# Optimization experiments

Measured on AMD Instinct MI355X. Metric: run time of the kernel, lower is better.

## Reference

```python
import jax, jax.numpy as jnp
import numpy as np

# Model dims (Gemma-class)
B, T, HID = 1, 3072, 2048
H, KH, D = 16, 8, 128          # q heads, kv heads, head_dim
WIN = 1024                     # sliding window
EPS = 1e-6
SEQ = 1536                     # two packed sequences of length 1536


def _rms(x, w):
    # torch nn.RMSNorm: x * rsqrt(mean(x^2) + eps) [* weight]
    var = jnp.mean(x * x, axis=-1, keepdims=True)
    y = x * jax.lax.rsqrt(var + EPS)
    return y if w is None else y * w


def _rotate_half(x):
    x1, x2 = jnp.split(x, 2, axis=-1)
    return jnp.concatenate([-x2, x1], axis=-1)


def _rope(x, cos, sin):
    # x: [B,T,h,D]; cos/sin: [B,T,rd] -> unsqueeze head dim (matches cos.unsqueeze(2))
    c = cos[:, :, None, :]
    s = sin[:, :, None, :]
    rd = cos.shape[-1]
    xr, xp = x[..., :rd], x[..., rd:]
    xr = xr * c + _rotate_half(xr) * s
    return jnp.concatenate([xr, xp], axis=-1)


def _build_mask(cu_seqlens):
    # causal & within sliding window & same packed sequence (matches _sliding_mask)
    idx = jnp.arange(T)
    seg = jnp.searchsorted(cu_seqlens, idx, side='right') - 1
    i = idx[:, None]
    j = idx[None, :]
    return (i >= j) & ((i - j) < WIN) & (seg[:, None] == seg[None, :])


def _attn_layer(x, wq, qn, k, v, wo, cos, sin, mask):
    # x: [B,T,HID]; k,v: [T,KH,D] (possibly shared from an earlier layer)
    q = _rope(_rms((x @ wq).reshape(B, T, H, D), qn), cos, sin).reshape(T, H, D)
    rep = H // k.shape[1]
    kk = jnp.repeat(k, rep, axis=1)   # GQA: repeat_interleave over head dim
    vv = jnp.repeat(v, rep, axis=1)
    s = jnp.einsum('qhd,khd->hqk', q, kk)          # scale = 1.0 (as in source)
    s = jnp.where(mask, s, jnp.asarray(-1e30, s.dtype))
    p = jax.nn.softmax(s, axis=-1)
    o = jnp.einsum('hqk,khd->qhd', p, vv).reshape(B, T, H * D)
    return o @ wo


def setup_inputs() -> dict:
    key = jax.random.key(0)
    ks = jax.random.split(key, 10)
    hidden_states = jax.random.normal(ks[0], (B, T, HID), jnp.float32)
    # RoPE tables with per-packed-sequence position resets
    pos = jnp.concatenate([jnp.arange(SEQ), jnp.arange(SEQ)]).astype(jnp.float32)
    inv = 1.0 / (10000.0 ** (jnp.arange(0, D, 2, dtype=jnp.float32) / D))
    fr = pos[:, None] * inv[None, :]
    emb = jnp.concatenate([fr, fr], axis=-1)     # [T, D]
    cos = jnp.cos(emb)[None]                     # [1, T, D]
    sin = jnp.sin(emb)[None]
    w = lambda k, sh: 0.02 * jax.random.normal(k, sh, jnp.float32)
    return {
        'hidden_states': hidden_states,
        'cos': cos, 'sin': sin,
        'wq0': w(ks[1], (HID, H * D)), 'wk0': w(ks[2], (HID, KH * D)),
        'wv0': w(ks[3], (HID, KH * D)), 'wo0': w(ks[4], (H * D, HID)),
        'qn0': 1.0 + 0.01 * jax.random.normal(ks[5], (D,), jnp.float32),
        'kn0': 1.0 + 0.01 * jax.random.normal(ks[6], (D,), jnp.float32),
        'wq1': w(ks[7], (HID, H * D)), 'wo1': w(ks[8], (H * D, HID)),
        'qn1': 1.0 + 0.01 * jax.random.normal(ks[9], (D,), jnp.float32),
        'cu_seqlens': jnp.array([0, SEQ, T], dtype=jnp.int32),
    }


def reference(hidden_states, cos, sin, wq0, wk0, wv0, wo0, qn0, kn0, wq1, wo1, qn1, cu_seqlens):
    mask = _build_mask(cu_seqlens)
    # Layer 0: source layer -> computes and stores K/V
    k = _rope(_rms((hidden_states @ wk0).reshape(B, T, KH, D), kn0), cos, sin).reshape(T, KH, D)
    v = _rms((hidden_states @ wv0).reshape(B, T, KH, D), None).reshape(T, KH, D)
    out0 = _attn_layer(hidden_states, wq0, qn0, k, v, wo0, cos, sin, mask)
    # Layer 1: KV-shared layer -> reuses layer 0's K/V (skips k/v projections)
    out1 = _attn_layer(out0, wq1, qn1, k, v, wo1, cos, sin, mask)
    return out1
```

## Files before the change

### kernel.cpp

```cpp
#include <hip/hip_runtime.h>
#include <hip/hip_bf16.h>

#define T_TOK 3072
#define HIDDEN 2048
#define NHQ 16
#define NHKV 8
#define DH 128
#define WINDOW 1024
#define KVN 1024

typedef __attribute__((ext_vector_type(4))) float f32x4;
typedef __attribute__((ext_vector_type(8))) short bf16x8;
typedef __attribute__((ext_vector_type(8))) unsigned short ushort8;
typedef __attribute__((ext_vector_type(4))) unsigned short ushort4v;

__device__ __forceinline__ unsigned short f2bf(float f) {
  union { float fv; unsigned u; } v; v.fv = f;
  unsigned r = v.u + 0x7fffu + ((v.u >> 16) & 1u);
  return (unsigned short)(r >> 16);
}
__device__ __forceinline__ float bf2f(unsigned short h) {
  union { unsigned u; float f; } v; v.u = ((unsigned)h) << 16;
  return v.f;
}
__device__ __forceinline__ void split2(float f, unsigned short& hi, unsigned short& lo) {
  hi = f2bf(f);
  lo = f2bf(f - bf2f(hi));
}

__global__ __launch_bounds__(256) void cvt_split(const float* __restrict__ x,
                                                 unsigned short* __restrict__ yh,
                                                 unsigned short* __restrict__ yl, int n) {
  int i = (blockIdx.x * 256 + threadIdx.x) * 4;
  if (i >= n) return;
  f32x4 v = *(const f32x4*)(x + i);
  ushort4v oh, ol;
#pragma unroll
  for (int j = 0; j < 4; ++j) {
    unsigned short h, l;
    split2(v[j], h, l);
    oh[j] = h; ol[j] = l;
  }
  *(ushort4v*)(yh + i) = oh;
  *(ushort4v*)(yl + i) = ol;
}

__global__ __launch_bounds__(256) void transpose_qkv(const float* __restrict__ wq0,
                                                     const float* __restrict__ wk0,
                                                     const float* __restrict__ wv0,
                                                     unsigned short* __restrict__ Wth,
                                                     unsigned short* __restrict__ Wtl) {
  __shared__ float tile[32][33];
  const int K = HIDDEN;
  int id = blockIdx.x;
  const float* W; int N, local; size_t dstoff;
  if (id < 4096)      { W = wq0; N = 2048; local = id;        dstoff = 0; }
  else if (id < 6144) { W = wk0; N = 1024; local = id - 4096; dstoff = (size_t)2048 * K; }
  else                { W = wv0; N = 1024; local = id - 6144; dstoff = (size_t)3072 * K; }
  int ntc = N / 32;
  int bn = (local % ntc) * 32, bk = (local / ntc) * 32;
  int tx = threadIdx.x & 31, ty = threadIdx.x >> 5;
#pragma unroll
  for (int i = 0; i < 4; ++i)
    tile[ty + i * 8][tx] = W[(size_t)(bk + ty + i * 8) * N + bn + tx];
  __syncthreads();
#pragma unroll
  for (int i = 0; i < 4; ++i) {
    unsigned short h, l;
    split2(tile[tx][ty + i * 8], h, l);
    Wth[dstoff + (size_t)(bn + ty + i * 8) * K + bk + tx] = h;
    Wtl[dstoff + (size_t)(bn + ty + i * 8) * K + bk + tx] = l;
  }
}

__global__ __launch_bounds__(256) void transpose_w_split(const float* __restrict__ W,
                                                         unsigned short* __restrict__ Wth,
                                                         unsigned short* __restrict__ Wtl,
                                                         int K, int N) {
  __shared__ float tile[32][33];
  int bn = blockIdx.x * 32, bk = blockIdx.y * 32;
  int tx = threadIdx.x & 31, ty = threadIdx.x >> 5;
#pragma unroll
  for (int i = 0; i < 4; ++i)
    tile[ty + i * 8][tx] = W[(size_t)(bk + ty + i * 8) * N + bn + tx];
  __syncthreads();
#pragma unroll
  for (int i = 0; i < 4; ++i) {
    unsigned short h, l;
    split2(tile[tx][ty + i * 8], h, l);
    Wth[(size_t)(bn + ty + i * 8) * K + bk + tx] = h;
    if (Wtl) Wtl[(size_t)(bn + ty + i * 8) * K + bk + tx] = l;
  }
}

__global__ __launch_bounds__(256) void transpose_u16(const unsigned short* __restrict__ src,
                                                     unsigned short* __restrict__ dst,
                                                     int R, int C) {
  __shared__ unsigned short tile[32][33];
  int bc = blockIdx.x * 32, br = blockIdx.y * 32;
  int tx = threadIdx.x & 31, ty = threadIdx.x >> 5;
#pragma unroll
  for (int i = 0; i < 4; ++i)
    tile[ty + i * 8][tx] = src[(size_t)(br + ty + i * 8) * C + bc + tx];
  __syncthreads();
#pragma unroll
  for (int i = 0; i < 4; ++i)
    dst[(size_t)(bc + ty + i * 8) * R + br + tx] = tile[tx][ty + i * 8];
}

#define GSLOT(lane) ((((lane) & 3) + 4 - (((lane) >> 3) & 3)) & 3)

template <int OUT>
__global__ __launch_bounds__(256) void gemm3_128(const unsigned short* __restrict__ Ah,
                                                 const unsigned short* __restrict__ Al,
                                                 const unsigned short* __restrict__ Bh,
                                                 const unsigned short* __restrict__ Bl,
                                                 float* __restrict__ Cq,
                                                 float* __restrict__ Ckv,
                                                 unsigned short* __restrict__ Ch,
                                                 unsigned short* __restrict__ Cl,
                                                 int strd, int M, int N, int K) {
  __shared__ unsigned short ah_lds[128 * 32];
  __shared__ unsigned short al_lds[128 * 32];
  __shared__ unsigned short bh_lds[128 * 32];
  __shared__ unsigned short bl_lds[128 * 32];
  const int tid = threadIdx.x, lane = tid & 63, wave = tid >> 6;
  const int wr = (wave >> 1) * 64, wc = (wave & 1) * 64;
  const int g = lane >> 4, r16 = lane & 15;
  int nwg = gridDim.x * gridDim.y;
  int id = blockIdx.y * gridDim.x + blockIdx.x;
  int nid = (id & 7) * (nwg >> 3) + (id >> 3);
  const int bm = nid % gridDim.x, bn = nid / gridDim.x;
  f32x4 acc[4][4];
#pragma unroll
  for (int i = 0; i < 4; ++i)
#pragma unroll
    for (int j = 0; j < 4; ++j) acc[i][j] = (f32x4){0.f, 0.f, 0.f, 0.f};

  const unsigned short* AhB = Ah + (size_t)bm * 128 * K;
  const unsigned short* AlB = Al + (size_t)bm * 128 * K;
  const unsigned short* BhB = Bh + (size_t)bn * 128 * K;
  const unsigned short* BlB = Bl + (size_t)bn * 128 * K;

  const int slg = GSLOT(lane) * 8;
  const int sr = ((r16 >> 1) & 3);

  for (int kt = 0; kt < K; kt += 32) {
    __syncthreads();
#pragma unroll
    for (int c = 0; c < 2; ++c) {
      size_t goff = (size_t)(wave * 32 + c * 16 + (lane >> 2)) * K + kt + slg;
      int loff = (wave * 2 + c) * 512;
      __builtin_amdgcn_global_load_lds(
          (const __attribute__((address_space(1))) unsigned int*)(AhB + goff),
          (__attribute__((address_space(3))) unsigned int*)(ah_lds + loff), 16, 0, 0);
      __builtin_amdgcn_global_load_lds(
          (const __attribute__((address_space(1))) unsigned int*)(AlB + goff),
          (__attribute__((address_space(3))) unsigned int*)(al_lds + loff), 16, 0, 0);
      __builtin_amdgcn_global_load_lds(
          (const __attribute__((address_space(1))) unsigned int*)(BhB + goff),
          (__attribute__((address_space(3))) unsigned int*)(bh_lds + loff), 16, 0, 0);
      __builtin_amdgcn_global_load_lds(
          (const __attribute__((address_space(1))) unsigned int*)(BlB + goff),
          (__attribute__((address_space(3))) unsigned int*)(bl_lds + loff), 16, 0, 0);
    }
    __syncthreads();
    bf16x8 ahf[4], alf[4], bhf[4], blf[4];
    int sa = ((g + sr) & 3) * 8;
#pragma unroll
    for (int i = 0; i < 4; ++i) {
      ahf[i] = *(const bf16x8*)&ah_lds[(wr + i * 16 + r16) * 32 + sa];
      alf[i] = *(const bf16x8*)&al_lds[(wr + i * 16 + r16) * 32 + sa];
      bhf[i] = *(const bf16x8*)&bh_lds[(wc + i * 16 + r16) * 32 + sa];
      blf[i] = *(const bf16x8*)&bl_lds[(wc + i * 16 + r16) * 32 + sa];
    }
#pragma unroll
    for (int i = 0; i < 4; ++i)
#pragma unroll
      for (int j = 0; j < 4; ++j) {
        acc[i][j] = __builtin_amdgcn_mfma_f32_16x16x32_bf16(ahf[i], bhf[j], acc[i][j], 0, 0, 0);
        acc[i][j] = __builtin_amdgcn_mfma_f32_16x16x32_bf16(ahf[i], blf[j], acc[i][j], 0, 0, 0);
        acc[i][j] = __builtin_amdgcn_mfma_f32_16x16x32_bf16(alf[i], bhf[j], acc[i][j], 0, 0, 0);
      }
  }

#pragma unroll
  for (int i = 0; i < 4; ++i) {
    int row = bm * 128 + wr + i * 16 + g * 4;
#pragma unroll
    for (int j = 0; j < 4; ++j) {
      int colg = bn * 128 + wc + j * 16 + r16;
      if (OUT == 0) {
        float* Cb; int cc;
        if (colg < 2048) { Cb = Cq; cc = colg; } else { Cb = Ckv; cc = colg - 2048; }
#pragma unroll
        for (int r = 0; r < 4; ++r)
          Cb[(size_t)(row + r) * strd + cc] = acc[i][j][r];
      } else {
#pragma unroll
        for (int r = 0; r < 4; ++r) {
          unsigned short h, l;
          split2(acc[i][j][r], h, l);
          Ch[(size_t)(row + r) * N + colg] = h;
          Cl[(size_t)(row + r) * N + colg] = l;
        }
      }
    }
  }
}

__global__ __launch_bounds__(256) void gemm3_96(const unsigned short* __restrict__ Ah,
                                                const unsigned short* __restrict__ Al,
                                                const unsigned short* __restrict__ Bh,
                                                const unsigned short* __restrict__ Bl,
                                                float* __restrict__ Cf,
                                                int M, int N, int K) {
  __shared__ unsigned short ah_lds[96 * 32];
  __shared__ unsigned short al_lds[96 * 32];
  __shared__ unsigned short bh_lds[128 * 32];
  __shared__ unsigned short bl_lds[128 * 32];
  const int tid = threadIdx.x, lane = tid & 63, wave = tid >> 6;
  const int wr = (wave >> 1) * 48, wc = (wave & 1) * 64;
  const int g = lane >> 4, r16 = lane & 15;
  int nwg = gridDim.x * gridDim.y;
  int id = blockIdx.y * gridDim.x + blockIdx.x;
  int nid = (id & 7) * (nwg >> 3) + (id >> 3);
  const int bm = nid % gridDim.x, bn = nid / gridDim.x;
  f32x4 acc[3][4];
#pragma unroll
  for (int i = 0; i < 3; ++i)
#pragma unroll
    for (int j = 0; j < 4; ++j) acc[i][j] = (f32x4){0.f, 0.f, 0.f, 0.f};

  const unsigned short* AhB = Ah + (size_t)bm * 96 * K;
  const unsigned short* AlB = Al + (size_t)bm * 96 * K;
  const unsigned short* BhB = Bh + (size_t)bn * 128 * K;
  const unsigned short* BlB = Bl + (size_t)bn * 128 * K;

  const int slg = GSLOT(lane) * 8;
  const int sr = ((r16 >> 1) & 3);

  for (int kt = 0; kt < K; kt += 32) {
    __syncthreads();
    {
      int c = wave;
      size_t goff = (size_t)(c * 16 + (lane >> 2)) * K + kt + slg;
      __builtin_amdgcn_global_load_lds(
          (const __attribute__((address_space(1))) unsigned int*)(AhB + goff),
          (__attribute__((address_space(3))) unsigned int*)(ah_lds + c * 512), 16, 0, 0);
      __builtin_amdgcn_global_load_lds(
          (const __attribute__((address_space(1))) unsigned int*)(AlB + goff),
          (__attribute__((address_space(3))) unsigned int*)(al_lds + c * 512), 16, 0, 0);
      if (wave < 2) {
        int c2 = 4 + wave;
        size_t goff2 = (size_t)(c2 * 16 + (lane >> 2)) * K + kt + slg;
        __builtin_amdgcn_global_load_lds(
            (const __attribute__((address_space(1))) unsigned int*)(AhB + goff2),
            (__attribute__((address_space(3))) unsigned int*)(ah_lds + c2 * 512), 16, 0, 0);
        __builtin_amdgcn_global_load_lds(
            (const __attribute__((address_space(1))) unsigned int*)(AlB + goff2),
            (__attribute__((address_space(3))) unsigned int*)(al_lds + c2 * 512), 16, 0, 0);
      }
    }
#pragma unroll
    for (int c = 0; c < 2; ++c) {
      size_t goff = (size_t)(wave * 32 + c * 16 + (lane >> 2)) * K + kt + slg;
      int loff = (wave * 2 + c) * 512;
      __builtin_amdgcn_global_load_lds(
          (const __attribute__((address_space(1))) unsigned int*)(BhB + goff),
          (__attribute__((address_space(3))) unsigned int*)(bh_lds + loff), 16, 0, 0);
      __builtin_amdgcn_global_load_lds(
          (const __attribute__((address_space(1))) unsigned int*)(BlB + goff),
          (__attribute__((address_space(3))) unsigned int*)(bl_lds + loff), 16, 0, 0);
    }
    __syncthreads();
    bf16x8 ahf[3], alf[3], bhf[4], blf[4];
    int sa = ((g + sr) & 3) * 8;
#pragma unroll
    for (int i = 0; i < 3; ++i) {
      ahf[i] = *(const bf16x8*)&ah_lds[(wr + i * 16 + r16) * 32 + sa];
      alf[i] = *(const bf16x8*)&al_lds[(wr + i * 16 + r16) * 32 + sa];
    }
#pragma unroll
    for (int j = 0; j < 4; ++j) {
      bhf[j] = *(const bf16x8*)&bh_lds[(wc + j * 16 + r16) * 32 + sa];
      blf[j] = *(const bf16x8*)&bl_lds[(wc + j * 16 + r16) * 32 + sa];
    }
#pragma unroll
    for (int i = 0; i < 3; ++i)
#pragma unroll
      for (int j = 0; j < 4; ++j) {
        acc[i][j] = __builtin_amdgcn_mfma_f32_16x16x32_bf16(ahf[i], bhf[j], acc[i][j], 0, 0, 0);
        acc[i][j] = __builtin_amdgcn_mfma_f32_16x16x32_bf16(ahf[i], blf[j], acc[i][j], 0, 0, 0);
        acc[i][j] = __builtin_amdgcn_mfma_f32_16x16x32_bf16(alf[i], bhf[j], acc[i][j], 0, 0, 0);
      }
  }

#pragma unroll
  for (int i = 0; i < 3; ++i) {
    int row = bm * 96 + wr + i * 16 + g * 4;
#pragma unroll
    for (int j = 0; j < 4; ++j) {
      int col = bn * 128 + wc + j * 16 + r16;
#pragma unroll
      for (int r = 0; r < 4; ++r)
        Cf[(size_t)(row + r) * N + col] = acc[i][j][r];
    }
  }
}

__global__ __launch_bounds__(256) void gemm1_96(const unsigned short* __restrict__ Ah,
                                                const unsigned short* __restrict__ Bh,
                                                float* __restrict__ Cf,
                                                int M, int N, int K) {
  __shared__ unsigned short ah_lds[96 * 32];
  __shared__ unsigned short bh_lds[128 * 32];
  const int tid = threadIdx.x, lane = tid & 63, wave = tid >> 6;
  const int wr = (wave >> 1) * 48, wc = (wave & 1) * 64;
  const int g = lane >> 4, r16 = lane & 15;
  int nwg = gridDim.x * gridDim.y;
  int id = blockIdx.y * gridDim.x + blockIdx.x;
  int nid = (id & 7) * (nwg >> 3) + (id >> 3);
  const int bm = nid % gridDim.x, bn = nid / gridDim.x;
  f32x4 acc[3][4];
#pragma unroll
  for (int i = 0; i < 3; ++i)
#pragma unroll
    for (int j = 0; j < 4; ++j) acc[i][j] = (f32x4){0.f, 0.f, 0.f, 0.f};

  const unsigned short* AhB = Ah + (size_t)bm * 96 * K;
  const unsigned short* BhB = Bh + (size_t)bn * 128 * K;

  const int slg = GSLOT(lane) * 8;
  const int sr = ((r16 >> 1) & 3);

  for (int kt = 0; kt < K; kt += 32) {
    __syncthreads();
    {
      int c = wave;
      size_t goff = (size_t)(c * 16 + (lane >> 2)) * K + kt + slg;
      __builtin_amdgcn_global_load_lds(
          (const __attribute__((address_space(1))) unsigned int*)(AhB + goff),
          (__attribute__((address_space(3))) unsigned int*)(ah_lds + c * 512), 16, 0, 0);
      if (wave < 2) {
        int c2 = 4 + wave;
        size_t goff2 = (size_t)(c2 * 16 + (lane >> 2)) * K + kt + slg;
        __builtin_amdgcn_global_load_lds(
            (const __attribute__((address_space(1))) unsigned int*)(AhB + goff2),
            (__attribute__((address_space(3))) unsigned int*)(ah_lds + c2 * 512), 16, 0, 0);
      }
    }
#pragma unroll
    for (int c = 0; c < 2; ++c) {
      size_t goff = (size_t)(wave * 32 + c * 16 + (lane >> 2)) * K + kt + slg;
      __builtin_amdgcn_global_load_lds(
          (const __attribute__((address_space(1))) unsigned int*)(BhB + goff),
          (__attribute__((address_space(3))) unsigned int*)(bh_lds + (wave * 2 + c) * 512), 16, 0, 0);
    }
    __syncthreads();
    bf16x8 ahf[3], bhf[4];
    int sa = ((g + sr) & 3) * 8;
#pragma unroll
    for (int i = 0; i < 3; ++i)
      ahf[i] = *(const bf16x8*)&ah_lds[(wr + i * 16 + r16) * 32 + sa];
#pragma unroll
    for (int j = 0; j < 4; ++j)
      bhf[j] = *(const bf16x8*)&bh_lds[(wc + j * 16 + r16) * 32 + sa];
#pragma unroll
    for (int i = 0; i < 3; ++i)
#pragma unroll
      for (int j = 0; j < 4; ++j)
        acc[i][j] = __builtin_amdgcn_mfma_f32_16x16x32_bf16(ahf[i], bhf[j], acc[i][j], 0, 0, 0);
  }

#pragma unroll
  for (int i = 0; i < 3; ++i) {
    int row = bm * 96 + wr + i * 16 + g * 4;
#pragma unroll
    for (int j = 0; j < 4; ++j) {
      int col = bn * 128 + wc + j * 16 + r16;
#pragma unroll
      for (int r = 0; r < 4; ++r)
        Cf[(size_t)(row + r) * N + col] = acc[i][j][r];
    }
  }
}

__global__ __launch_bounds__(256) void rms_kv(const float* __restrict__ X,
                                              const float* __restrict__ kn,
                                              const float* __restrict__ cosp,
                                              const float* __restrict__ sinp,
                                              unsigned short* __restrict__ kh,
                                              unsigned short* __restrict__ kl,
                                              unsigned short* __restrict__ vh) {
  const int half = T_TOK * NHKV / 4;
  bool isV = (int)blockIdx.x >= half;
  int bid = isV ? blockIdx.x - half : blockIdx.x;
  int row = bid * 4 + (threadIdx.x >> 6);
  int lane = threadIdx.x & 63;
  int t = row >> 3, hh_ = row & 7;
  const float* x = X + (size_t)t * HIDDEN + (isV ? KVN : 0) + (size_t)hh_ * DH;
  float x1 = x[lane], x2 = x[lane + 64];
  float ss = x1 * x1 + x2 * x2;
#pragma unroll
  for (int m = 1; m < 64; m <<= 1) ss += __shfl_xor(ss, m, 64);
  float inv = rsqrtf(ss * (1.0f / 128.0f) + 1e-6f);
  float y1 = x1 * inv, y2 = x2 * inv;
  if (!isV) {
    y1 *= kn[lane]; y2 *= kn[lane + 64];
    float c1 = cosp[t * DH + lane], s1 = sinp[t * DH + lane];
    float c2 = cosp[t * DH + lane + 64], s2 = sinp[t * DH + lane + 64];
    float o1 = y1 * c1 - y2 * s1;
    float o2 = y2 * c2 + y1 * s2;
    unsigned short h, l;
    split2(o1, h, l);
    kh[(size_t)row * DH + lane] = h;
    kl[(size_t)row * DH + lane] = l;
    split2(o2, h, l);
    kh[(size_t)row * DH + lane + 64] = h;
    kl[(size_t)row * DH + lane + 64] = l;
  } else {
    vh[(size_t)row * DH + lane] = f2bf(y1);
    vh[(size_t)row * DH + lane + 64] = f2bf(y2);
  }
}

template <int WRITE_LO>
__global__ __launch_bounds__(384) void attn3(const float* __restrict__ Qf,
                                             const float* __restrict__ qnw,
                                             const float* __restrict__ cosp,
                                             const float* __restrict__ sinp,
                                             const unsigned short* __restrict__ Kh,
                                             const unsigned short* __restrict__ Kl,
                                             const unsigned short* __restrict__ Vth,
                                             unsigned short* __restrict__ Oh,
                                             unsigned short* __restrict__ Ol,
                                             const int* __restrict__ cu, int ncu) {
  __shared__ unsigned short kh_lds[32][136];
  __shared__ unsigned short kl_lds[32][136];
  __shared__ unsigned short vh_lds[144][40];
  __shared__ unsigned short ph_lds[6][16][40];

  int id = blockIdx.y * gridDim.x + blockIdx.x;
  int nid = (id & 7) * 64 + (id >> 3);
  const int qt = nid & 31, h = nid >> 5;
  const int qbase = qt * 96;
  const int kvh = h >> 1;
  const int tid = threadIdx.x, lane = tid & 63, wave = tid >> 6;
  const int g = lane >> 4, r16 = lane & 15;

  for (int i = tid; i < 16 * 40; i += 384) {
    int rr = i / 40, cc = i % 40;
    vh_lds[128 + rr][cc] = (rr == 0) ? (unsigned short)0x3F80 : (unsigned short)0;
  }

  bf16x8 aqh[4], aql[4];
  {
    int q_r = qbase + wave * 16 + r16;
    const float* xq = Qf + (size_t)q_r * HIDDEN + h * DH;
    float xv[4][8];
    float ss = 0.f;
#pragma unroll
    for (int ks = 0; ks < 4; ++ks) {
      f32x4 a = *(const f32x4*)(xq + ks * 32 + g * 8);
      f32x4 b = *(const f32x4*)(xq + ks * 32 + g * 8 + 4);
#pragma unroll
      for (int j = 0; j < 4; ++j) { xv[ks][j] = a[j]; xv[ks][4 + j] = b[j]; }
#pragma unroll
      for (int j = 0; j < 8; ++j) ss += xv[ks][j] * xv[ks][j];
    }
    ss += __shfl_xor(ss, 16, 64);
    ss += __shfl_xor(ss, 32, 64);
    float inv = rsqrtf(ss * (1.0f / 128.0f) + 1e-6f);
    float y[4][8];
#pragma unroll
    for (int ks = 0; ks < 4; ++ks) {
      f32x4 w0 = *(const f32x4*)(qnw + ks * 32 + g * 8);
      f32x4 w1 = *(const f32x4*)(qnw + ks * 32 + g * 8 + 4);
#pragma unroll
      for (int j = 0; j < 4; ++j) {
        y[ks][j] = xv[ks][j] * inv * w0[j];
        y[ks][4 + j] = xv[ks][4 + j] * inv * w1[j];
      }
    }
    const float* cb = cosp + (size_t)q_r * DH;
    const float* sb = sinp + (size_t)q_r * DH;
#pragma unroll
    for (int ks = 0; ks < 4; ++ks) {
      bf16x8 th, tl;
#pragma unroll
      for (int j2 = 0; j2 < 2; ++j2) {
        int col = ks * 32 + g * 8 + j2 * 4;
        f32x4 cv = *(const f32x4*)(cb + col);
        f32x4 sv = *(const f32x4*)(sb + col);
#pragma unroll
        for (int j = 0; j < 4; ++j) {
          float o;
          if (ks < 2) o = y[ks][j2 * 4 + j] * cv[j] - y[ks + 2][j2 * 4 + j] * sv[j];
          else        o = y[ks][j2 * 4 + j] * cv[j] + y[ks - 2][j2 * 4 + j] * sv[j];
          unsigned short hx, lx;
          split2(o, hx, lx);
          th[j2 * 4 + j] = (short)hx;
          tl[j2 * 4 + j] = (short)lx;
        }
      }
      aqh[ks] = th; aql[ks] = tl;
    }
  }

  int ssr[4];
#pragma unroll
  for (int r = 0; r < 4; ++r) {
    int q_r = qbase + wave * 16 + g * 4 + r;
    int s = 0;
    for (int i = 1; i < ncu; ++i) { int v = cu[i]; if (v <= q_r) s = v; }
    ssr[r] = s;
  }
  int ss_base = 0;
  for (int i = 1; i < ncu; ++i) { int v = cu[i]; if (v <= qbase) ss_base = v; }

  float m_r[4] = {-1e30f, -1e30f, -1e30f, -1e30f};
  f32x4 oacc[8];
#pragma unroll
  for (int db = 0; db < 8; ++db) oacc[db] = (f32x4){0.f, 0.f, 0.f, 0.f};
  f32x4 oaccL = (f32x4){0.f, 0.f, 0.f, 0.f};

  int lo = qbase - WINDOW + 1;
  if (lo < ss_base) lo = ss_base;
  if (lo < 0) lo = 0;
  int kt0 = lo & ~31;
  int ktend = qbase + 95;

  const bool stager = tid < 256;
  const int krow = (tid & 255) >> 3, kc = tid & 7;
  const int vd = (tid & 255) >> 1, vhalf = (tid & 1) * 16;
  const int qmin = qbase + wave * 16;
  const int sw0 = ((kc + 2 * (krow & 15)) & 15) * 16;
  const int sw1 = ((kc + 8 + 2 * (krow & 15)) & 15) * 16;

  ushort8 rkh0, rkh1, rkl0, rkl1, rvh0, rvh1;
  auto loadTile = [&](int kt) {
    if (!stager) return;
    size_t goff = ((size_t)(kt + krow) * NHKV + kvh) * DH + kc * 8;
    rkh0 = *(const ushort8*)(Kh + goff);
    rkh1 = *(const ushort8*)(Kh + goff + 64);
    rkl0 = *(const ushort8*)(Kl + goff);
    rkl1 = *(const ushort8*)(Kl + goff + 64);
    size_t voff = ((size_t)kvh * DH + vd) * T_TOK + kt + vhalf;
    rvh0 = *(const ushort8*)(Vth + voff);
    rvh1 = *(const ushort8*)(Vth + voff + 8);
  };
  auto writeTile = [&]() {
    if (!stager) return;
    char* kbh = (char*)&kh_lds[krow][0];
    char* kbl = (char*)&kl_lds[krow][0];
    *(ushort8*)(kbh + sw0) = rkh0;
    *(ushort8*)(kbh + sw1) = rkh1;
    *(ushort8*)(kbl + sw0) = rkl0;
    *(ushort8*)(kbl + sw1) = rkl1;
    *(ushort8*)&vh_lds[vd][vhalf] = rvh0;
    *(ushort8*)&vh_lds[vd][vhalf + 8] = rvh1;
  };

  loadTile(kt0);
  writeTile();
  __syncthreads();

  for (int kt = kt0; kt <= ktend; kt += 32) {
    const bool hasNext = (kt + 32 <= ktend);
    if (hasNext) loadTile(kt + 32);

    f32x4 s0 = (f32x4){0.f, 0.f, 0.f, 0.f}, s1 = (f32x4){0.f, 0.f, 0.f, 0.f};
    {
      const char* kb0h = (const char*)&kh_lds[r16][0];
      const char* kb1h = (const char*)&kh_lds[16 + r16][0];
      const char* kb0l = (const char*)&kl_lds[r16][0];
      const char* kb1l = (const char*)&kl_lds[16 + r16][0];
#pragma unroll
      for (int ks = 0; ks < 4; ++ks) {
        int sl = ((ks * 4 + g + 2 * r16) & 15) * 16;
        bf16x8 bh0 = *(const bf16x8*)(kb0h + sl);
        bf16x8 bh1 = *(const bf16x8*)(kb1h + sl);
        bf16x8 bl0 = *(const bf16x8*)(kb0l + sl);
        bf16x8 bl1 = *(const bf16x8*)(kb1l + sl);
        s0 = __builtin_amdgcn_mfma_f32_16x16x32_bf16(aqh[ks], bh0, s0, 0, 0, 0);
        s0 = __builtin_amdgcn_mfma_f32_16x16x32_bf16(aqh[ks], bl0, s0, 0, 0, 0);
        s0 = __builtin_amdgcn_mfma_f32_16x16x32_bf16(aql[ks], bh0, s0, 0, 0, 0);
        s1 = __builtin_amdgcn_mfma_f32_16x16x32_bf16(aqh[ks], bh1, s1, 0, 0, 0);
        s1 = __builtin_amdgcn_mfma_f32_16x16x32_bf16(aqh[ks], bl1, s1, 0, 0, 0);
        s1 = __builtin_amdgcn_mfma_f32_16x16x32_bf16(aql[ks], bh1, s1, 0, 0, 0);
      }
    }

    float sv0_[4], sv1_[4], mt_[4];
    bool ok0_[4], ok1_[4];
    bool interior = (kt + 31 <= qmin) && (kt >= qmin + 16 - WINDOW) &&
                    __all(kt >= ssr[3]);
    if (interior) {
#pragma unroll
      for (int r = 0; r < 4; ++r) {
        ok0_[r] = ok1_[r] = true;
        sv0_[r] = s0[r]; sv1_[r] = s1[r];
      }
    } else {
#pragma unroll
      for (int r = 0; r < 4; ++r) {
        int q_r = qmin + g * 4 + r;
        int k0 = kt + r16, k1 = k0 + 16;
        ok0_[r] = (k0 <= q_r) && (k0 > q_r - WINDOW) && (k0 >= ssr[r]);
        ok1_[r] = (k1 <= q_r) && (k1 > q_r - WINDOW) && (k1 >= ssr[r]);
        sv0_[r] = ok0_[r] ? s0[r] : -1e30f;
        sv1_[r] = ok1_[r] ? s1[r] : -1e30f;
      }
    }
#pragma unroll
    for (int r = 0; r < 4; ++r) {
      float mt = fmaxf(sv0_[r], sv1_[r]);
#pragma unroll
      for (int mm = 1; mm < 16; mm <<= 1) mt = fmaxf(mt, __shfl_xor(mt, mm, 64));
      mt_[r] = mt;
    }
    float grow = fmaxf(fmaxf(mt_[0] - m_r[0], mt_[1] - m_r[1]),
                       fmaxf(mt_[2] - m_r[2], mt_[3] - m_r[3]));
    if (!__all(grow <= 8.0f)) {
#pragma unroll
      for (int r = 0; r < 4; ++r) {
        float mnew = fmaxf(m_r[r], mt_[r]);
        float alpha = __expf(m_r[r] - mnew);
        m_r[r] = mnew;
#pragma unroll
        for (int db = 0; db < 8; ++db) oacc[db][r] *= alpha;
        oaccL[r] *= alpha;
      }
    }
#pragma unroll
    for (int r = 0; r < 4; ++r) {
      float p0v = ok0_[r] ? __expf(sv0_[r] - m_r[r]) : 0.f;
      float p1v = ok1_[r] ? __expf(sv1_[r] - m_r[r]) : 0.f;
      ph_lds[wave][g * 4 + r][r16] = f2bf(p0v);
      ph_lds[wave][g * 4 + r][16 + r16] = f2bf(p1v);
    }

    bf16x8 pah = *(const bf16x8*)&ph_lds[wave][r16][g * 8];
#pragma unroll
    for (int db = 0; db < 8; ++db) {
      bf16x8 vfh = *(const bf16x8*)&vh_lds[db * 16 + r16][g * 8];
      oacc[db] = __builtin_amdgcn_mfma_f32_16x16x32_bf16(pah, vfh, oacc[db], 0, 0, 0);
    }
    {
      bf16x8 vfo = *(const bf16x8*)&vh_lds[128 + r16][g * 8];
      oaccL = __builtin_amdgcn_mfma_f32_16x16x32_bf16(pah, vfo, oaccL, 0, 0, 0);
    }

    __syncthreads();
    if (hasNext) writeTile();
    __syncthreads();
  }

#pragma unroll
  for (int r = 0; r < 4; ++r) {
    int q_r = qbase + wave * 16 + g * 4 + r;
    float lsum = __shfl(oaccL[r], lane & 48, 64);
    float invl = 1.f / lsum;
#pragma unroll
    for (int db = 0; db < 8; ++db) {
      float ov = oacc[db][r] * invl;
      unsigned short hh, ll;
      split2(ov, hh, ll);
      Oh[(size_t)q_r * (NHQ * DH) + h * DH + db * 16 + r16] = hh;
      if (WRITE_LO) Ol[(size_t)q_r * (NHQ * DH) + h * DH + db * 16 + r16] = ll;
    }
  }
}

extern "C" void kernel_launch(void* const* d_in, const int* in_sizes, int n_in,
                              void* d_out, int out_size, void* d_ws, size_t ws_size,
                              hipStream_t stream) {
  const float* hidden = (const float*)d_in[0];
  const float* cosp   = (const float*)d_in[1];
  const float* sinp   = (const float*)d_in[2];
  const float* wq0    = (const float*)d_in[3];
  const float* wk0    = (const float*)d_in[4];
  const float* wv0    = (const float*)d_in[5];
  const float* wo0    = (const float*)d_in[6];
  const float* qn0    = (const float*)d_in[7];
  const float* kn0    = (const float*)d_in[8];
  const float* wq1    = (const float*)d_in[9];
  const float* wo1    = (const float*)d_in[10];
  const float* qn1    = (const float*)d_in[11];
  const int*   cu     = (const int*)d_in[12];
  int ncu = in_sizes[12];
  (void)n_in; (void)out_size; (void)ws_size;

  const int nX = T_TOK * HIDDEN;

  char* p = (char*)d_ws;
  auto alloc = [&](size_t bytes) { char* r = p; p += (bytes + 255) & ~255ull; return r; };

  float*          c32q  = (float*)alloc((size_t)T_TOK * HIDDEN * 4);
  float*          c32kv = (float*)alloc((size_t)T_TOK * HIDDEN * 4);
  unsigned short* xh    = (unsigned short*)alloc((size_t)T_TOK * HIDDEN * 2);
  unsigned short* xl    = (unsigned short*)alloc((size_t)T_TOK * HIDDEN * 2);
  unsigned short* wth   = (unsigned short*)alloc((size_t)2 * HIDDEN * HIDDEN * 2);
  unsigned short* wtl   = (unsigned short*)alloc((size_t)2 * HIDDEN * HIDDEN * 2);
  unsigned short* kh    = (unsigned short*)alloc((size_t)T_TOK * KVN * 2);
  unsigned short* kl    = (unsigned short*)alloc((size_t)T_TOK * KVN * 2);
  unsigned short* vh    = (unsigned short*)alloc((size_t)T_TOK * KVN * 2);
  unsigned short* vth   = (unsigned short*)alloc((size_t)T_TOK * KVN * 2);

  unsigned short* wo0sh = wth;
  unsigned short* wo0sl = wtl;
  unsigned short* wq1th = wth + (size_t)HIDDEN * HIDDEN;
  unsigned short* wq1tl = wtl + (size_t)HIDDEN * HIDDEN;
  unsigned short* W01th = (unsigned short*)c32q;
  unsigned short* W01tl = W01th + (size_t)HIDDEN * HIDDEN;
  unsigned short* wo1t  = wth;

  cvt_split<<<nX / 1024, 256, 0, stream>>>(hidden, xh, xl, nX);

  transpose_qkv<<<8192, 256, 0, stream>>>(wq0, wk0, wv0, wth, wtl);

  gemm3_128<0><<<dim3(T_TOK / 128, 4096 / 128), 256, 0, stream>>>(
      xh, xl, wth, wtl, c32q, c32kv, nullptr, nullptr, HIDDEN, T_TOK, 4096, HIDDEN);

  cvt_split<<<(HIDDEN * HIDDEN) / 1024, 256, 0, stream>>>(wo0, wo0sh, wo0sl, HIDDEN * HIDDEN);

  transpose_w_split<<<dim3(HIDDEN / 32, HIDDEN / 32), 256, 0, stream>>>(wq1, wq1th, wq1tl, HIDDEN, HIDDEN);

  rms_kv<<<2 * T_TOK * NHKV / 4, 256, 0, stream>>>(c32kv, kn0, cosp, sinp, kh, kl, vh);

  transpose_u16<<<dim3(KVN / 32, T_TOK / 32), 256, 0, stream>>>(vh, vth, T_TOK, KVN);

  attn3<1><<<dim3(32, 16), 384, 0, stream>>>(c32q, qn0, cosp, sinp, kh, kl, vth, xh, xl, cu, ncu);

  gemm3_128<2><<<dim3(HIDDEN / 128, HIDDEN / 128), 256, 0, stream>>>(
      wq1th, wq1tl, wo0sh, wo0sl, nullptr, nullptr, W01th, W01tl, HIDDEN, HIDDEN, HIDDEN, HIDDEN);

  gemm3_96<<<dim3(T_TOK / 96, HIDDEN / 128), 256, 0, stream>>>(
      xh, xl, W01th, W01tl, c32kv, T_TOK, HIDDEN, HIDDEN);

  transpose_w_split<<<dim3(HIDDEN / 32, HIDDEN / 32), 256, 0, stream>>>(wo1, wo1t, nullptr, HIDDEN, HIDDEN);

  attn3<0><<<dim3(32, 16), 384, 0, stream>>>(c32kv, qn1, cosp, sinp, kh, kl, vth, xh, nullptr, cu, ncu);

  gemm1_96<<<dim3(T_TOK / 96, HIDDEN / 128), 256, 0, stream>>>(xh, wo1t, (float*)d_out, T_TOK, HIDDEN, HIDDEN);
}
```

Measured before the change: 666.6 us.

## Give each attention wave two 16-row query tiles, 128-row blocks with 256 threads

The attention kernel now processes 128 query rows per block with 4 waves of 256 threads, each wave handling two 16-row query sub-tiles instead of one. Every K/V tile loaded into LDS is reused across twice as many query rows per wave, and all threads now take part in staging (previously a third of the threads idled during loads). The cost is about double the accumulator registers per wave, which lowers occupancy, and a smaller grid of 384 blocks, which may underfill the 256 CUs.

After: 795.3 us. 19.3% more time.

```diff
diff --git a/kernel.cpp b/kernel.cpp
--- a/kernel.cpp
+++ b/kernel.cpp
@@ -426,7 +426,7 @@
 }
 
 template <int WRITE_LO>
-__global__ __launch_bounds__(384) void attn3(const float* __restrict__ Qf,
+__global__ __launch_bounds__(256) void attn3(const float* __restrict__ Qf,
                                              const float* __restrict__ qnw,
                                              const float* __restrict__ cosp,
                                              const float* __restrict__ sinp,
@@ -439,24 +439,25 @@
   __shared__ unsigned short kh_lds[32][136];
   __shared__ unsigned short kl_lds[32][136];
   __shared__ unsigned short vh_lds[144][40];
-  __shared__ unsigned short ph_lds[6][16][40];
+  __shared__ unsigned short ph_lds[4][32][40];
 
   int id = blockIdx.y * gridDim.x + blockIdx.x;
-  int nid = (id & 7) * 64 + (id >> 3);
-  const int qt = nid & 31, h = nid >> 5;
-  const int qbase = qt * 96;
+  int nid = (id & 7) * 48 + (id >> 3);
+  const int qt = nid % 24, h = nid / 24;
+  const int qbase = qt * 128;
   const int kvh = h >> 1;
   const int tid = threadIdx.x, lane = tid & 63, wave = tid >> 6;
   const int g = lane >> 4, r16 = lane & 15;
 
-  for (int i = tid; i < 16 * 40; i += 384) {
+  for (int i = tid; i < 16 * 40; i += 256) {
     int rr = i / 40, cc = i % 40;
     vh_lds[128 + rr][cc] = (rr == 0) ? (unsigned short)0x3F80 : (unsigned short)0;
   }
 
-  bf16x8 aqh[4], aql[4];
-  {
-    int q_r = qbase + wave * 16 + r16;
+  bf16x8 aqh[2][4], aql[2][4];
+#pragma unroll
+  for (int hf = 0; hf < 2; ++hf) {
+    int q_r = qbase + wave * 32 + hf * 16 + r16;
     const float* xq = Qf + (size_t)q_r * HIDDEN + h * DH;
     float xv[4][8];
     float ss = 0.f;
@@ -472,15 +473,14 @@
     ss += __shfl_xor(ss, 16, 64);
     ss += __shfl_xor(ss, 32, 64);
     float inv = rsqrtf(ss * (1.0f / 128.0f) + 1e-6f);
-    float y[4][8];
 #pragma unroll
     for (int ks = 0; ks < 4; ++ks) {
       f32x4 w0 = *(const f32x4*)(qnw + ks * 32 + g * 8);
       f32x4 w1 = *(const f32x4*)(qnw + ks * 32 + g * 8 + 4);
 #pragma unroll
       for (int j = 0; j < 4; ++j) {
-        y[ks][j] = xv[ks][j] * inv * w0[j];
-        y[ks][4 + j] = xv[ks][4 + j] * inv * w1[j];
+        xv[ks][j] = xv[ks][j] * inv * w0[j];
+        xv[ks][4 + j] = xv[ks][4 + j] * inv * w1[j];
       }
     }
     const float* cb = cosp + (size_t)q_r * DH;
@@ -496,51 +496,59 @@
 #pragma unroll
         for (int j = 0; j < 4; ++j) {
           float o;
-          if (ks < 2) o = y[ks][j2 * 4 + j] * cv[j] - y[ks + 2][j2 * 4 + j] * sv[j];
-          else        o = y[ks][j2 * 4 + j] * cv[j] + y[ks - 2][j2 * 4 + j] * sv[j];
+          if (ks < 2) o = xv[ks][j2 * 4 + j] * cv[j] - xv[ks + 2][j2 * 4 + j] * sv[j];
+          else        o = xv[ks][j2 * 4 + j] * cv[j] + xv[ks - 2][j2 * 4 + j] * sv[j];
           unsigned short hx, lx;
           split2(o, hx, lx);
           th[j2 * 4 + j] = (short)hx;
           tl[j2 * 4 + j] = (short)lx;
         }
       }
-      aqh[ks] = th; aql[ks] = tl;
-    }
-  }
-
-  int ssr[4];
-#pragma unroll
-  for (int r = 0; r < 4; ++r) {
-    int q_r = qbase + wave * 16 + g * 4 + r;
-    int s = 0;
-    for (int i = 1; i < ncu; ++i) { int v = cu[i]; if (v <= q_r) s = v; }
-    ssr[r] = s;
-  }
+      aqh[hf][ks] = th; aql[hf][ks] = tl;
+    }
+  }
+
+  int ssr[2][4];
+#pragma unroll
+  for (int hf = 0; hf < 2; ++hf)
+#pragma unroll
+    for (int r = 0; r < 4; ++r) {
+      int q_r = qbase + wave * 32 + hf * 16 + g * 4 + r;
+      int s = 0;
+      for (int i = 1; i < ncu; ++i) { int v = cu[i]; if (v <= q_r) s = v; }
+      ssr[hf][r] = s;
+    }
   int ss_base = 0;
   for (int i = 1; i < ncu; ++i) { int v = cu[i]; if (v <= qbase) ss_base = v; }
 
-  float m_r[4] = {-1e30f, -1e30f, -1e30f, -1e30f};
-  f32x4 oacc[8];
-#pragma unroll
-  for (int db = 0; db < 8; ++db) oacc[db] = (f32x4){0.f, 0.f, 0.f, 0.f};
-  f32x4 oaccL = (f32x4){0.f, 0.f, 0.f, 0.f};
+  float m_r[2][4];
+#pragma unroll
+  for (int hf = 0; hf < 2; ++hf)
+#pragma unroll
+    for (int r = 0; r < 4; ++r) m_r[hf][r] = -1e30f;
+  f32x4 oaccA[8], oaccB[8];
+#pragma unroll
+  for (int db = 0; db < 8; ++db) {
+    oaccA[db] = (f32x4){0.f, 0.f, 0.f, 0.f};
+    oaccB[db] = (f32x4){0.f, 0.f, 0.f, 0.f};
+  }
+  f32x4 oaccLA = (f32x4){0.f, 0.f, 0.f, 0.f};
+  f32x4 oaccLB = (f32x4){0.f, 0.f, 0.f, 0.f};
 
   int lo = qbase - WINDOW + 1;
   if (lo < ss_base) lo = ss_base;
   if (lo < 0) lo = 0;
   int kt0 = lo & ~31;
-  int ktend = qbase + 95;
-
-  const bool stager = tid < 256;
-  const int krow = (tid & 255) >> 3, kc = tid & 7;
-  const int vd = (tid & 255) >> 1, vhalf = (tid & 1) * 16;
-  const int qmin = qbase + wave * 16;
+  int ktend = qbase + 127;
+
+  const int krow = tid >> 3, kc = tid & 7;
+  const int vd = tid >> 1, vhalf = (tid & 1) * 16;
+  const int qmin = qbase + wave * 32;
   const int sw0 = ((kc + 2 * (krow & 15)) & 15) * 16;
   const int sw1 = ((kc + 8 + 2 * (krow & 15)) & 15) * 16;
 
   ushort8 rkh0, rkh1, rkl0, rkl1, rvh0, rvh1;
   auto loadTile = [&](int kt) {
-    if (!stager) return;
     size_t goff = ((size_t)(kt + krow) * NHKV + kvh) * DH + kc * 8;
     rkh0 = *(const ushort8*)(Kh + goff);
     rkh1 = *(const ushort8*)(Kh + goff + 64);
@@ -551,7 +559,6 @@
     rvh1 = *(const ushort8*)(Vth + voff + 8);
   };
   auto writeTile = [&]() {
-    if (!stager) return;
     char* kbh = (char*)&kh_lds[krow][0];
     char* kbl = (char*)&kl_lds[krow][0];
     *(ushort8*)(kbh + sw0) = rkh0;
@@ -570,7 +577,8 @@
     const bool hasNext = (kt + 32 <= ktend);
     if (hasNext) loadTile(kt + 32);
 
-    f32x4 s0 = (f32x4){0.f, 0.f, 0.f, 0.f}, s1 = (f32x4){0.f, 0.f, 0.f, 0.f};
+    f32x4 s0a = (f32x4){0.f, 0.f, 0.f, 0.f}, s1a = (f32x4){0.f, 0.f, 0.f, 0.f};
+    f32x4 s0b = (f32x4){0.f, 0.f, 0.f, 0.f}, s1b = (f32x4){0.f, 0.f, 0.f, 0.f};
     {
       const char* kb0h = (const char*)&kh_lds[r16][0];
       const char* kb1h = (const char*)&kh_lds[16 + r16][0];
@@ -583,73 +591,94 @@
         bf16x8 bh1 = *(const bf16x8*)(kb1h + sl);
         bf16x8 bl0 = *(const bf16x8*)(kb0l + sl);
         bf16x8 bl1 = *(const bf16x8*)(kb1l + sl);
-        s0 = __builtin_amdgcn_mfma_f32_16x16x32_bf16(aqh[ks], bh0, s0, 0, 0, 0);
-        s0 = __builtin_amdgcn_mfma_f32_16x16x32_bf16(aqh[ks], bl0, s0, 0, 0, 0);
-        s0 = __builtin_amdgcn_mfma_f32_16x16x32_bf16(aql[ks], bh0, s0, 0, 0, 0);
-        s1 = __builtin_amdgcn_mfma_f32_16x16x32_bf16(aqh[ks], bh1, s1, 0, 0, 0);
-        s1 = __builtin_amdgcn_mfma_f32_16x16x32_bf16(aqh[ks], bl1, s1, 0, 0, 0);
-        s1 = __builtin_amdgcn_mfma_f32_16x16x32_bf16(aql[ks], bh1, s1, 0, 0, 0);
-      }
-    }
-
-    float sv0_[4], sv1_[4], mt_[4];
-    bool ok0_[4], ok1_[4];
-    bool interior = (kt + 31 <= qmin) && (kt >= qmin + 16 - WINDOW) &&
-                    __all(kt >= ssr[3]);
-    if (interior) {
+        s0a = __builtin_amdgcn_mfma_f32_16x16x32_bf16(aqh[0][ks], bh0, s0a, 0, 0, 0);
+        s0a = __builtin_amdgcn_mfma_f32_16x16x32_bf16(aqh[0][ks], bl0, s0a, 0, 0, 0);
+        s0a = __builtin_amdgcn_mfma_f32_16x16x32_bf16(aql[0][ks], bh0, s0a, 0, 0, 0);
+        s1a = __builtin_amdgcn_mfma_f32_16x16x32_bf16(aqh[0][ks], bh1, s1a, 0, 0, 0);
+        s1a = __builtin_amdgcn_mfma_f32_16x16x32_bf16(aqh[0][ks], bl1, s1a, 0, 0, 0);
+        s1a = __builtin_amdgcn_mfma_f32_16x16x32_bf16(aql[0][ks], bh1, s1a, 0, 0, 0);
+        s0b = __builtin_amdgcn_mfma_f32_16x16x32_bf16(aqh[1][ks], bh0, s0b, 0, 0, 0);
+        s0b = __builtin_amdgcn_mfma_f32_16x16x32_bf16(aqh[1][ks], bl0, s0b, 0, 0, 0);
+        s0b = __builtin_amdgcn_mfma_f32_16x16x32_bf16(aql[1][ks], bh0, s0b, 0, 0, 0);
+        s1b = __builtin_amdgcn_mfma_f32_16x16x32_bf16(aqh[1][ks], bh1, s1b, 0, 0, 0);
+        s1b = __builtin_amdgcn_mfma_f32_16x16x32_bf16(aqh[1][ks], bl1, s1b, 0, 0, 0);
+        s1b = __builtin_amdgcn_mfma_f32_16x16x32_bf16(aql[1][ks], bh1, s1b, 0, 0, 0);
+      }
+    }
+
+#pragma unroll
+    for (int hf = 0; hf < 2; ++hf) {
+      f32x4 s0 = hf ? s0b : s0a;
+      f32x4 s1 = hf ? s1b : s1a;
+      float sv0_[4], sv1_[4], mt_[4];
+      bool ok0_[4], ok1_[4];
+      int qminh = qmin + hf * 16;
+      bool interior = (kt + 31 <= qminh) && (kt >= qminh + 16 - WINDOW) &&
+                      __all(kt >= ssr[hf][3]);
+      if (interior) {
+#pragma unroll
+        for (int r = 0; r < 4; ++r) {
+          ok0_[r] = ok1_[r] = true;
+          sv0_[r] = s0[r]; sv1_[r] = s1[r];
+        }
+      } else {
+#pragma unroll
+        for (int r = 0; r < 4; ++r) {
+          int q_r = qminh + g * 4 + r;
+          int k0 = kt + r16, k1 = k0 + 16;
+          ok0_[r] = (k0 <= q_r) && (k0 > q_r - WINDOW) && (k0 >= ssr[hf][r]);
+          ok1_[r] = (k1 <= q_r) && (k1 > q_r - WINDOW) && (k1 >= ssr[hf][r]);
+          sv0_[r] = ok0_[r] ? s0[r] : -1e30f;
+          sv1_[r] = ok1_[r] ? s1[r] : -1e30f;
+        }
+      }
 #pragma unroll
       for (int r = 0; r < 4; ++r) {
-        ok0_[r] = ok1_[r] = true;
-        sv0_[r] = s0[r]; sv1_[r] = s1[r];
-      }
-    } else {
+        float mt = fmaxf(sv0_[r], sv1_[r]);
+#pragma unroll
+        for (int mm = 1; mm < 16; mm <<= 1) mt = fmaxf(mt, __shfl_xor(mt, mm, 64));
+        mt_[r] = mt;
+      }
+      float grow = fmaxf(fmaxf(mt_[0] - m_r[hf][0], mt_[1] - m_r[hf][1]),
+                         fmaxf(mt_[2] - m_r[hf][2], mt_[3] - m_r[hf][3]));
+      if (!__all(grow <= 8.0f)) {
+#pragma unroll
+        for (int r = 0; r < 4; ++r) {
+          float mnew = fmaxf(m_r[hf][r], mt_[r]);
+          float alpha = __expf(m_r[hf][r] - mnew);
+          m_r[hf][r] = mnew;
+          if (hf == 0) {
+#pragma unroll
+            for (int db = 0; db < 8; ++db) oaccA[db][r] *= alpha;
+            oaccLA[r] *= alpha;
+          } else {
+#pragma unroll
+            for (int db = 0; db < 8; ++db) oaccB[db][r] *= alpha;
+            oaccLB[r] *= alpha;
+          }
+        }
+      }
 #pragma unroll
       for (int r = 0; r < 4; ++r) {
-        int q_r = qmin + g * 4 + r;
-        int k0 = kt + r16, k1 = k0 + 16;
-        ok0_[r] = (k0 <= q_r) && (k0 > q_r - WINDOW) && (k0 >= ssr[r]);
-        ok1_[r] = (k1 <= q_r) && (k1 > q_r - WINDOW) && (k1 >= ssr[r]);
-        sv0_[r] = ok0_[r] ? s0[r] : -1e30f;
-        sv1_[r] = ok1_[r] ? s1[r] : -1e30f;
-      }
-    }
-#pragma unroll
-    for (int r = 0; r < 4; ++r) {
-      float mt = fmaxf(sv0_[r], sv1_[r]);
-#pragma unroll
-      for (int mm = 1; mm < 16; mm <<= 1) mt = fmaxf(mt, __shfl_xor(mt, mm, 64));
-      mt_[r] = mt;
-    }
-    float grow = fmaxf(fmaxf(mt_[0] - m_r[0], mt_[1] - m_r[1]),
-                       fmaxf(mt_[2] - m_r[2], mt_[3] - m_r[3]));
-    if (!__all(grow <= 8.0f)) {
-#pragma unroll
-      for (int r = 0; r < 4; ++r) {
-        float mnew = fmaxf(m_r[r], mt_[r]);
-        float alpha = __expf(m_r[r] - mnew);
-        m_r[r] = mnew;
-#pragma unroll
-        for (int db = 0; db < 8; ++db) oacc[db][r] *= alpha;
-        oaccL[r] *= alpha;
-      }
-    }
-#pragma unroll
-    for (int r = 0; r < 4; ++r) {
-      float p0v = ok0_[r] ? __expf(sv0_[r] - m_r[r]) : 0.f;
-      float p1v = ok1_[r] ? __expf(sv1_[r] - m_r[r]) : 0.f;
-      ph_lds[wave][g * 4 + r][r16] = f2bf(p0v);
-      ph_lds[wave][g * 4 + r][16 + r16] = f2bf(p1v);
-    }
-
-    bf16x8 pah = *(const bf16x8*)&ph_lds[wave][r16][g * 8];
+        float p0v = ok0_[r] ? __expf(sv0_[r] - m_r[hf][r]) : 0.f;
+        float p1v = ok1_[r] ? __expf(sv1_[r] - m_r[hf][r]) : 0.f;
+        ph_lds[wave][hf * 16 + g * 4 + r][r16] = f2bf(p0v);
+        ph_lds[wave][hf * 16 + g * 4 + r][16 + r16] = f2bf(p1v);
+      }
+    }
+
+    bf16x8 pa0 = *(const bf16x8*)&ph_lds[wave][r16][g * 8];
+    bf16x8 pa1 = *(const bf16x8*)&ph_lds[wave][16 + r16][g * 8];
 #pragma unroll
     for (int db = 0; db < 8; ++db) {
       bf16x8 vfh = *(const bf16x8*)&vh_lds[db * 16 + r16][g * 8];
-      oacc[db] = __builtin_amdgcn_mfma_f32_16x16x32_bf16(pah, vfh, oacc[db], 0, 0, 0);
+      oaccA[db] = __builtin_amdgcn_mfma_f32_16x16x32_bf16(pa0, vfh, oaccA[db], 0, 0, 0);
+      oaccB[db] = __builtin_amdgcn_mfma_f32_16x16x32_bf16(pa1, vfh, oaccB[db], 0, 0, 0);
     }
     {
       bf16x8 vfo = *(const bf16x8*)&vh_lds[128 + r16][g * 8];
-      oaccL = __builtin_amdgcn_mfma_f32_16x16x32_bf16(pah, vfo, oaccL, 0, 0, 0);
+      oaccLA = __builtin_amdgcn_mfma_f32_16x16x32_bf16(pa0, vfo, oaccLA, 0, 0, 0);
+      oaccLB = __builtin_amdgcn_mfma_f32_16x16x32_bf16(pa1, vfo, oaccLB, 0, 0, 0);
     }
 
     __syncthreads();
@@ -658,17 +687,20 @@
   }
 
 #pragma unroll
-  for (int r = 0; r < 4; ++r) {
-    int q_r = qbase + wave * 16 + g * 4 + r;
-    float lsum = __shfl(oaccL[r], lane & 48, 64);
-    float invl = 1.f / lsum;
-#pragma unroll
-    for (int db = 0; db < 8; ++db) {
-      float ov = oacc[db][r] * invl;
-      unsigned short hh, ll;
-      split2(ov, hh, ll);
-      Oh[(size_t)q_r * (NHQ * DH) + h * DH + db * 16 + r16] = hh;
-      if (WRITE_LO) Ol[(size_t)q_r * (NHQ * DH) + h * DH + db * 16 + r16] = ll;
+  for (int hf = 0; hf < 2; ++hf) {
+#pragma unroll
+    for (int r = 0; r < 4; ++r) {
+      int q_r = qbase + wave * 32 + hf * 16 + g * 4 + r;
+      float lsum = __shfl(hf ? oaccLB[r] : oaccLA[r], lane & 48, 64);
+      float invl = 1.f / lsum;
+#pragma unroll
+      for (int db = 0; db < 8; ++db) {
+        float ov = (hf ? oaccB[db][r] : oaccA[db][r]) * invl;
+        unsigned short hh, ll;
+        split2(ov, hh, ll);
+        Oh[(size_t)q_r * (NHQ * DH) + h * DH + db * 16 + r16] = hh;
+        if (WRITE_LO) Ol[(size_t)q_r * (NHQ * DH) + h * DH + db * 16 + r16] = ll;
+      }
     }
   }
 }
@@ -717,31 +749,19 @@
   unsigned short* wo1t  = wth;
 
   cvt_split<<<nX / 1024, 256, 0, stream>>>(hidden, xh, xl, nX);
-
   transpose_qkv<<<8192, 256, 0, stream>>>(wq0, wk0, wv0, wth, wtl);
-
   gemm3_128<0><<<dim3(T_TOK / 128, 4096 / 128), 256, 0, stream>>>(
       xh, xl, wth, wtl, c32q, c32kv, nullptr, nullptr, HIDDEN, T_TOK, 4096, HIDDEN);
-
   cvt_split<<<(HIDDEN * HIDDEN) / 1024, 256, 0, stream>>>(wo0, wo0sh, wo0sl, HIDDEN * HIDDEN);
-
   transpose_w_split<<<dim3(HIDDEN / 32, HIDDEN / 32), 256, 0, stream>>>(wq1, wq1th, wq1tl, HIDDEN, HIDDEN);
-
   rms_kv<<<2 * T_TOK * NHKV / 4, 256, 0, stream>>>(c32kv, kn0, cosp, sinp, kh, kl, vh);
-
   transpose_u16<<<dim3(KVN / 32, T_TOK / 32), 256, 0, stream>>>(vh, vth, T_TOK, KVN);
-
-  attn3<1><<<dim3(32, 16), 384, 0, stream>>>(c32q, qn0, cosp, sinp, kh, kl, vth, xh, xl, cu, ncu);
-
+  attn3<1><<<dim3(24, 16), 256, 0, stream>>>(c32q, qn0, cosp, sinp, kh, kl, vth, xh, xl, cu, ncu);
   gemm3_128<2><<<dim3(HIDDEN / 128, HIDDEN / 128), 256, 0, stream>>>(
       wq1th, wq1tl, wo0sh, wo0sl, nullptr, nullptr, W01th, W01tl, HIDDEN, HIDDEN, HIDDEN, HIDDEN);
-
   gemm3_96<<<dim3(T_TOK / 96, HIDDEN / 128), 256, 0, stream>>>(
       xh, xl, W01th, W01tl, c32kv, T_TOK, HIDDEN, HIDDEN);
-
   transpose_w_split<<<dim3(HIDDEN / 32, HIDDEN / 32), 256, 0, stream>>>(wo1, wo1t, nullptr, HIDDEN, HIDDEN);
-
-  attn3<0><<<dim3(32, 16), 384, 0, stream>>>(c32kv, qn1, cosp, sinp, kh, kl, vth, xh, nullptr, cu, ncu);
-
+  attn3<0><<<dim3(24, 16), 256, 0, stream>>>(c32kv, qn1, cosp, sinp, kh, kl, vth, xh, nullptr, cu, ncu);
   gemm1_96<<<dim3(T_TOK / 96, HIDDEN / 128), 256, 0, stream>>>(xh, wo1t, (float*)d_out, T_TOK, HIDDEN, HIDDEN);
 }
```
